# Performance work log

Measured on AMD Instinct MI355X. Metric: run time of the kernel, lower is better.

## Reference

```python
import jax, jax.numpy as jnp
import numpy as np

# H36M-style 17-joint skeleton: bones[b] = (parent_joint, child_joint)
BONES = [(0,1),(1,2),(2,3),(0,4),(4,5),(5,6),(0,7),(7,8),(8,9),(9,10),
         (8,11),(11,12),(12,13),(8,14),(14,15),(15,16)]
N_JOINTS = 17
ROOT = 0


def _euler_xyz_to_matrix(e):
    # pytorch3d euler_angles_to_matrix(e, 'XYZ'): R = Rx(a) @ Ry(b) @ Rz(c)
    cx, cy, cz = jnp.cos(e[..., 0]), jnp.cos(e[..., 1]), jnp.cos(e[..., 2])
    sx, sy, sz = jnp.sin(e[..., 0]), jnp.sin(e[..., 1]), jnp.sin(e[..., 2])
    one, zero = jnp.ones_like(cx), jnp.zeros_like(cx)
    shp = e.shape[:-1] + (3, 3)
    Rx = jnp.stack([one, zero, zero, zero, cx, -sx, zero, sx, cx], -1).reshape(shp)
    Ry = jnp.stack([cy, zero, sy, zero, one, zero, -sy, zero, cy], -1).reshape(shp)
    Rz = jnp.stack([cz, -sz, zero, sz, cz, zero, zero, zero, one], -1).reshape(shp)
    return Rx @ Ry @ Rz


def setup_inputs() -> dict:
    key = jax.random.key(0)
    k1, k2 = jax.random.split(key)
    N = 500000
    euler_angle = jax.random.normal(k1, (N, 16, 3), dtype=jnp.float32)
    bone_length = jax.random.uniform(k2, (N, 16, 1), dtype=jnp.float32)
    return {"euler_angle": euler_angle, "bone_length": bone_length}


def reference(euler_angle, bone_length):
    # euler_angle: (N, 16, 3), bone_length: (N, 16, 1)
    N = euler_angle.shape[0]
    R = _euler_xyz_to_matrix(euler_angle)  # (N, 16, 3, 3)
    # Accumulated rotations in pytorch3d row-vector convention: p' = p @ M,
    # compose(M_parent, R_i) -> M_parent @ R_i.
    M = [None] * N_JOINTS
    pos = [None] * N_JOINTS
    M[ROOT] = jnp.broadcast_to(jnp.eye(3, dtype=euler_angle.dtype), (N, 3, 3))
    pos[ROOT] = jnp.zeros((N, 3), dtype=euler_angle.dtype)
    for i, (j0, j1) in enumerate(BONES):
        M[j1] = jnp.einsum('nij,njk->nik', M[j0], R[:, i])
        # local offset is (0, 0, L) so p @ M == L * M[:, 2, :] (third row)
        pos[j1] = bone_length[:, i, 0, None] * M[j1][:, 2, :] + pos[j0]
    return jnp.stack(pos, axis=1)  # (N, 17, 3)
```

## Files before the change

kernel.cpp:

```cpp
#include <hip/hip_runtime.h>


#define NB 64

__device__ __forceinline__ void mm3(const float A[9], const float B[9], float C[9]) {
#pragma unroll
    for (int r = 0; r < 3; ++r) {
        C[3*r+0] = A[3*r+0]*B[0] + A[3*r+1]*B[3] + A[3*r+2]*B[6];
        C[3*r+1] = A[3*r+0]*B[1] + A[3*r+1]*B[4] + A[3*r+2]*B[7];
        C[3*r+2] = A[3*r+0]*B[2] + A[3*r+1]*B[5] + A[3*r+2]*B[8];
    }
}

__device__ __forceinline__ void euler_rot(const float* __restrict__ ev, int i, float R[9]) {
    float a = ev[3*i+0], b = ev[3*i+1], c = ev[3*i+2];
    float sx, cx, sy, cy, sz, cz;
    __sincosf(a, &sx, &cx);
    __sincosf(b, &sy, &cy);
    __sincosf(c, &sz, &cz);
    R[0] = cy*cz;             R[1] = -cy*sz;            R[2] = sy;
    R[3] = sx*sy*cz + cx*sz;  R[4] = -sx*sy*sz + cx*cz; R[5] = -sx*cy;
    R[6] = -cx*sy*cz + sx*sz; R[7] = cx*sy*sz + sx*cz;  R[8] = cx*cy;
}

__global__ void __launch_bounds__(NB, 3)
fk17_kernel(const float* __restrict__ euler, const float* __restrict__ blen,
            float* __restrict__ out, int n)
{
    __shared__ float s_o[NB * 51];

    const int tid    = threadIdx.x;
    const int block0 = blockIdx.x * NB;
    const int nvalid = min(NB, n - block0);
    const int t      = block0 + tid;

    if (tid < nvalid) {
        float ev[48];
        const float4* ge4 = (const float4*)(euler + (size_t)t * 48);
#pragma unroll
        for (int q = 0; q < 12; ++q) {
            float4 v = ge4[q];
            ev[4*q+0] = v.x; ev[4*q+1] = v.y; ev[4*q+2] = v.z; ev[4*q+3] = v.w;
        }
        float L[16];
        const float4* gb4 = (const float4*)(blen + (size_t)t * 16);
#pragma unroll
        for (int q = 0; q < 4; ++q) {
            float4 v = gb4[q];
            L[4*q+0] = v.x; L[4*q+1] = v.y; L[4*q+2] = v.z; L[4*q+3] = v.w;
        }

        float* o = s_o + tid * 51;
        float Ma[9], Mb[9], M8[9], R[9];
        float px, py, pz, p8x, p8y, p8z;

        o[0] = 0.f; o[1] = 0.f; o[2] = 0.f;

        euler_rot(ev, 0, Ma);
        px = L[0]*Ma[6]; py = L[0]*Ma[7]; pz = L[0]*Ma[8];
        o[3] = px; o[4] = py; o[5] = pz;
        euler_rot(ev, 1, R); mm3(Ma, R, Mb);
        px += L[1]*Mb[6]; py += L[1]*Mb[7]; pz += L[1]*Mb[8];
        o[6] = px; o[7] = py; o[8] = pz;
        euler_rot(ev, 2, R); mm3(Mb, R, Ma);
        px += L[2]*Ma[6]; py += L[2]*Ma[7]; pz += L[2]*Ma[8];
        o[9] = px; o[10] = py; o[11] = pz;

        euler_rot(ev, 3, Ma);
        px = L[3]*Ma[6]; py = L[3]*Ma[7]; pz = L[3]*Ma[8];
        o[12] = px; o[13] = py; o[14] = pz;
        euler_rot(ev, 4, R); mm3(Ma, R, Mb);
        px += L[4]*Mb[6]; py += L[4]*Mb[7]; pz += L[4]*Mb[8];
        o[15] = px; o[16] = py; o[17] = pz;
        euler_rot(ev, 5, R); mm3(Mb, R, Ma);
        px += L[5]*Ma[6]; py += L[5]*Ma[7]; pz += L[5]*Ma[8];
        o[18] = px; o[19] = py; o[20] = pz;

        euler_rot(ev, 6, Ma);
        px = L[6]*Ma[6]; py = L[6]*Ma[7]; pz = L[6]*Ma[8];
        o[21] = px; o[22] = py; o[23] = pz;
        euler_rot(ev, 7, R); mm3(Ma, R, M8);
        px += L[7]*M8[6]; py += L[7]*M8[7]; pz += L[7]*M8[8];
        o[24] = px; o[25] = py; o[26] = pz;
        p8x = px; p8y = py; p8z = pz;

        euler_rot(ev, 8, R); mm3(M8, R, Ma);
        px = p8x + L[8]*Ma[6]; py = p8y + L[8]*Ma[7]; pz = p8z + L[8]*Ma[8];
        o[27] = px; o[28] = py; o[29] = pz;
        euler_rot(ev, 9, R); mm3(Ma, R, Mb);
        px += L[9]*Mb[6]; py += L[9]*Mb[7]; pz += L[9]*Mb[8];
        o[30] = px; o[31] = py; o[32] = pz;

        euler_rot(ev, 10, R); mm3(M8, R, Ma);
        px = p8x + L[10]*Ma[6]; py = p8y + L[10]*Ma[7]; pz = p8z + L[10]*Ma[8];
        o[33] = px; o[34] = py; o[35] = pz;
        euler_rot(ev, 11, R); mm3(Ma, R, Mb);
        px += L[11]*Mb[6]; py += L[11]*Mb[7]; pz += L[11]*Mb[8];
        o[36] = px; o[37] = py; o[38] = pz;
        euler_rot(ev, 12, R); mm3(Mb, R, Ma);
        px += L[12]*Ma[6]; py += L[12]*Ma[7]; pz += L[12]*Ma[8];
        o[39] = px; o[40] = py; o[41] = pz;

        euler_rot(ev, 13, R); mm3(M8, R, Ma);
        px = p8x + L[13]*Ma[6]; py = p8y + L[13]*Ma[7]; pz = p8z + L[13]*Ma[8];
        o[42] = px; o[43] = py; o[44] = pz;
        euler_rot(ev, 14, R); mm3(Ma, R, Mb);
        px += L[14]*Mb[6]; py += L[14]*Mb[7]; pz += L[14]*Mb[8];
        o[45] = px; o[46] = py; o[47] = pz;
        euler_rot(ev, 15, R); mm3(Mb, R, Ma);
        px += L[15]*Ma[6]; py += L[15]*Ma[7]; pz += L[15]*Ma[8];
        o[48] = px; o[49] = py; o[50] = pz;
    }
    __syncthreads();

    if (nvalid == NB) {
        const float4* so4 = (const float4*)s_o;
        float4*       og4 = (float4*)(out + (size_t)block0 * 51);
#pragma unroll
        for (int k = 0; k < 13; ++k) {
            int i4 = tid + 64 * k;
            if (k < 12 || i4 < 816) og4[i4] = so4[i4];
        }
    } else {
        float* og = out + (size_t)block0 * 51;
        const int tot = nvalid * 51;
        for (int i = tid; i < tot; i += NB)
            og[i] = s_o[i];
    }
}

extern "C" void kernel_launch(void* const* d_in, const int* in_sizes, int n_in,
                              void* d_out, int out_size, void* d_ws, size_t ws_size,
                              hipStream_t stream) {
    const float* euler = (const float*)d_in[0];
    const float* blen  = (const float*)d_in[1];
    float* out = (float*)d_out;

    const int n    = in_sizes[0] / 48;
    const int grid = (n + NB - 1) / NB;
    fk17_kernel<<<grid, NB, 0, stream>>>(euler, blen, out, n);
}
```

Before: 200.2 us.

## Stage euler angles into LDS with coalesced direct global-to-LDS loads

Euler angles are now loaded cooperatively with `__builtin_amdgcn_global_load_lds`, written straight into a padded LDS buffer (52 floats per sample). Each thread then reads its angles from LDS. This replaces the per-thread 192-byte-strided float4 loads, which coalesce poorly. The same LDS buffer is reused in place for the output, and the write-back now uses scalar coalesced stores that skip the padding, replacing the earlier float4 stores. The costs are an extra explicit vmcnt wait, a barrier before compute, a dummy 13th chunk loaded per sample, and more store instructions.

```diff
diff --git a/kernel.cpp b/kernel.cpp
--- a/kernel.cpp
+++ b/kernel.cpp
@@ -2,6 +2,9 @@
 
 
 #define NB 64
+
+#define GLB_PTR(x) ((const __attribute__((address_space(1))) void*)(x))
+#define LDS_PTR(x) ((__attribute__((address_space(3))) void*)(x))
 
 __device__ __forceinline__ void mm3(const float A[9], const float B[9], float C[9]) {
 #pragma unroll
@@ -12,8 +15,7 @@
     }
 }
 
-__device__ __forceinline__ void euler_rot(const float* __restrict__ ev, int i, float R[9]) {
-    float a = ev[3*i+0], b = ev[3*i+1], c = ev[3*i+2];
+__device__ __forceinline__ void erot(float a, float b, float c, float R[9]) {
     float sx, cx, sy, cy, sz, cz;
     __sincosf(a, &sx, &cx);
     __sincosf(b, &sy, &cy);
@@ -27,105 +29,136 @@
 fk17_kernel(const float* __restrict__ euler, const float* __restrict__ blen,
             float* __restrict__ out, int n)
 {
-    __shared__ float s_o[NB * 51];
+    __shared__ float s_b[NB * 52];
 
     const int tid    = threadIdx.x;
     const int block0 = blockIdx.x * NB;
     const int nvalid = min(NB, n - block0);
     const int t      = block0 + tid;
+    const int tc     = min(t, n - 1);
 
-    if (tid < nvalid) {
-        float ev[48];
-        const float4* ge4 = (const float4*)(euler + (size_t)t * 48);
 #pragma unroll
-        for (int q = 0; q < 12; ++q) {
-            float4 v = ge4[q];
-            ev[4*q+0] = v.x; ev[4*q+1] = v.y; ev[4*q+2] = v.z; ev[4*q+3] = v.w;
-        }
-        float L[16];
-        const float4* gb4 = (const float4*)(blen + (size_t)t * 16);
+    for (int j = 0; j < 13; ++j) {
+        int m = j * 64 + tid;
+        int s = m / 13;
+        int c = m - s * 13;
+        if (c == 12) c = 0;
+        int gs = min(block0 + s, n - 1);
+        __builtin_amdgcn_global_load_lds(
+            GLB_PTR(euler + (size_t)gs * 48 + c * 4),
+            LDS_PTR(s_b + j * 256), 16, 0, 0);
+    }
+
+    float L[16];
+    {
+        const float4* gb4 = (const float4*)(blen + (size_t)tc * 16);
 #pragma unroll
         for (int q = 0; q < 4; ++q) {
             float4 v = gb4[q];
             L[4*q+0] = v.x; L[4*q+1] = v.y; L[4*q+2] = v.z; L[4*q+3] = v.w;
         }
+    }
 
-        float* o = s_o + tid * 51;
+    asm volatile("s_waitcnt vmcnt(0)" ::: "memory");
+    __syncthreads();
+
+    if (tid < nvalid) {
+        float* o = s_b + tid * 52;
+        float ex, ey, ez, fx, fy, fz;
         float Ma[9], Mb[9], M8[9], R[9];
         float px, py, pz, p8x, p8y, p8z;
 
+        ex = o[0];  ey = o[1];  ez = o[2];
+        fx = o[3];  fy = o[4];  fz = o[5];
         o[0] = 0.f; o[1] = 0.f; o[2] = 0.f;
 
-        euler_rot(ev, 0, Ma);
+        erot(ex, ey, ez, Ma);
         px = L[0]*Ma[6]; py = L[0]*Ma[7]; pz = L[0]*Ma[8];
+        ex = o[6];  ey = o[7];  ez = o[8];
         o[3] = px; o[4] = py; o[5] = pz;
-        euler_rot(ev, 1, R); mm3(Ma, R, Mb);
+        erot(fx, fy, fz, R); mm3(Ma, R, Mb);
         px += L[1]*Mb[6]; py += L[1]*Mb[7]; pz += L[1]*Mb[8];
+        fx = o[9];  fy = o[10]; fz = o[11];
         o[6] = px; o[7] = py; o[8] = pz;
-        euler_rot(ev, 2, R); mm3(Mb, R, Ma);
+        erot(ex, ey, ez, R); mm3(Mb, R, Ma);
         px += L[2]*Ma[6]; py += L[2]*Ma[7]; pz += L[2]*Ma[8];
+        ex = o[12]; ey = o[13]; ez = o[14];
         o[9] = px; o[10] = py; o[11] = pz;
 
-        euler_rot(ev, 3, Ma);
+        erot(fx, fy, fz, Ma);
         px = L[3]*Ma[6]; py = L[3]*Ma[7]; pz = L[3]*Ma[8];
+        fx = o[15]; fy = o[16]; fz = o[17];
         o[12] = px; o[13] = py; o[14] = pz;
-        euler_rot(ev, 4, R); mm3(Ma, R, Mb);
+        erot(ex, ey, ez, R); mm3(Ma, R, Mb);
         px += L[4]*Mb[6]; py += L[4]*Mb[7]; pz += L[4]*Mb[8];
+        ex = o[18]; ey = o[19]; ez = o[20];
         o[15] = px; o[16] = py; o[17] = pz;
-        euler_rot(ev, 5, R); mm3(Mb, R, Ma);
+        erot(fx, fy, fz, R); mm3(Mb, R, Ma);
         px += L[5]*Ma[6]; py += L[5]*Ma[7]; pz += L[5]*Ma[8];
+        fx = o[21]; fy = o[22]; fz = o[23];
         o[18] = px; o[19] = py; o[20] = pz;
 
-        euler_rot(ev, 6, Ma);
+        erot(ex, ey, ez, Ma);
         px = L[6]*Ma[6]; py = L[6]*Ma[7]; pz = L[6]*Ma[8];
+        ex = o[24]; ey = o[25]; ez = o[26];
         o[21] = px; o[22] = py; o[23] = pz;
-        euler_rot(ev, 7, R); mm3(Ma, R, M8);
+        erot(fx, fy, fz, R); mm3(Ma, R, M8);
         px += L[7]*M8[6]; py += L[7]*M8[7]; pz += L[7]*M8[8];
+        fx = o[27]; fy = o[28]; fz = o[29];
         o[24] = px; o[25] = py; o[26] = pz;
         p8x = px; p8y = py; p8z = pz;
 
-        euler_rot(ev, 8, R); mm3(M8, R, Ma);
+        erot(ex, ey, ez, R); mm3(M8, R, Ma);
         px = p8x + L[8]*Ma[6]; py = p8y + L[8]*Ma[7]; pz = p8z + L[8]*Ma[8];
+        ex = o[30]; ey = o[31]; ez = o[32];
         o[27] = px; o[28] = py; o[29] = pz;
-        euler_rot(ev, 9, R); mm3(Ma, R, Mb);
+        erot(fx, fy, fz, R); mm3(Ma, R, Mb);
         px += L[9]*Mb[6]; py += L[9]*Mb[7]; pz += L[9]*Mb[8];
+        fx = o[33]; fy = o[34]; fz = o[35];
         o[30] = px; o[31] = py; o[32] = pz;
 
-        euler_rot(ev, 10, R); mm3(M8, R, Ma);
+        erot(ex, ey, ez, R); mm3(M8, R, Ma);
         px = p8x + L[10]*Ma[6]; py = p8y + L[10]*Ma[7]; pz = p8z + L[10]*Ma[8];
+        ex = o[36]; ey = o[37]; ez = o[38];
         o[33] = px; o[34] = py; o[35] = pz;
-        euler_rot(ev, 11, R); mm3(Ma, R, Mb);
+        erot(fx, fy, fz, R); mm3(Ma, R, Mb);
         px += L[11]*Mb[6]; py += L[11]*Mb[7]; pz += L[11]*Mb[8];
+        fx = o[39]; fy = o[40]; fz = o[41];
         o[36] = px; o[37] = py; o[38] = pz;
-        euler_rot(ev, 12, R); mm3(Mb, R, Ma);
+        erot(ex, ey, ez, R); mm3(Mb, R, Ma);
         px += L[12]*Ma[6]; py += L[12]*Ma[7]; pz += L[12]*Ma[8];
+        ex = o[42]; ey = o[43]; ez = o[44];
         o[39] = px; o[40] = py; o[41] = pz;
 
-        euler_rot(ev, 13, R); mm3(M8, R, Ma);
+        erot(fx, fy, fz, R); mm3(M8, R, Ma);
         px = p8x + L[13]*Ma[6]; py = p8y + L[13]*Ma[7]; pz = p8z + L[13]*Ma[8];
+        fx = o[45]; fy = o[46]; fz = o[47];
         o[42] = px; o[43] = py; o[44] = pz;
-        euler_rot(ev, 14, R); mm3(Ma, R, Mb);
+        erot(ex, ey, ez, R); mm3(Ma, R, Mb);
         px += L[14]*Mb[6]; py += L[14]*Mb[7]; pz += L[14]*Mb[8];
         o[45] = px; o[46] = py; o[47] = pz;
-        euler_rot(ev, 15, R); mm3(Mb, R, Ma);
+        erot(fx, fy, fz, R); mm3(Mb, R, Ma);
         px += L[15]*Ma[6]; py += L[15]*Ma[7]; pz += L[15]*Ma[8];
         o[48] = px; o[49] = py; o[50] = pz;
     }
     __syncthreads();
 
-    if (nvalid == NB) {
-        const float4* so4 = (const float4*)s_o;
-        float4*       og4 = (float4*)(out + (size_t)block0 * 51);
+    {
+        float* og = out + (size_t)block0 * 51;
+        if (nvalid == NB) {
 #pragma unroll
-        for (int k = 0; k < 13; ++k) {
-            int i4 = tid + 64 * k;
-            if (k < 12 || i4 < 816) og4[i4] = so4[i4];
+            for (int k = 0; k < 51; ++k) {
+                int m = tid + 64 * k;
+                int s = m / 51;
+                og[m] = s_b[m + s];
+            }
+        } else {
+            const int tot = nvalid * 51;
+            for (int m = tid; m < tot; m += NB) {
+                int s = m / 51;
+                og[m] = s_b[m + s];
+            }
         }
-    } else {
-        float* og = out + (size_t)block0 * 51;
-        const int tot = nvalid * 51;
-        for (int i = tid; i < tot; i += NB)
-            og[i] = s_o[i];
     }
 }
 
```

New measurement: 200.3 us. No clear change (+0.1%).
